# Optimization experiments

Hardware: AMD Instinct MI355X
Metric: run time of the kernel (lower is better)

The kernel has to match this reference:

```python
import jax, jax.numpy as jnp
import numpy as np

NUM_HEADS = 16
EPS = 1e-6

def _rmsnorm(h, w):
    h32 = h.astype(jnp.float32)
    var = jnp.mean(h32 * h32, axis=-1, keepdims=True)
    return (w * (h32 * jax.lax.rsqrt(var + EPS))).astype(h.dtype)

def setup_inputs() -> dict:
    key = jax.random.key(0)
    ks = jax.random.split(key, 4)
    B, N, C = 16, 1024, 1024
    x = jax.random.normal(ks[0], (B, N, C), dtype=jnp.float32)
    qkv_w = jax.random.normal(ks[1], (3 * C, C), dtype=jnp.float32) * (C ** -0.5)
    proj_w = jax.random.normal(ks[2], (C, C), dtype=jnp.float32) * (C ** -0.5)
    proj_b = jnp.zeros((C,), dtype=jnp.float32)
    q_norm_w = jnp.ones((C // NUM_HEADS,), dtype=jnp.float32)
    k_norm_w = jnp.ones((C // NUM_HEADS,), dtype=jnp.float32)
    return {"x": x, "qkv_w": qkv_w, "proj_w": proj_w, "proj_b": proj_b,
            "q_norm_w": q_norm_w, "k_norm_w": k_norm_w}

def reference(x, qkv_w, proj_w, proj_b, q_norm_w, k_norm_w):
    B, N, C = x.shape
    H = NUM_HEADS
    Dh = C // H
    scale = Dh ** -0.5  # qk_scale default; temperature = 1.0
    # QKV projection (no bias): [B,N,3,H,Dh]
    qkv = (x @ qkv_w.T).reshape(B, N, 3, H, Dh)
    q, k, v = qkv[:, :, 0], qkv[:, :, 1], qkv[:, :, 2]
    # per-head QK RMSNorm (fp32 internally)
    q = _rmsnorm(q, q_norm_w)
    k = _rmsnorm(k, k_norm_w)
    # explicit softmax attention: [B,H,N,N]
    attn = jnp.einsum('bnhd,bmhd->bhnm', q * scale, k)
    attn = jax.nn.softmax(attn, axis=-1)
    out = jnp.einsum('bhnm,bmhd->bnhd', attn, v).reshape(B, N, C)
    return out @ proj_w.T + proj_b
```

## Files before the change

### kernel.cpp

```cpp
#include <hip/hip_runtime.h>
#include <hip/hip_bf16.h>

typedef __attribute__((ext_vector_type(8))) __bf16 bf16x8;
typedef __attribute__((ext_vector_type(4))) __bf16 bf16x4;
typedef __attribute__((ext_vector_type(4))) float f32x4;

#define AS1(p) ((__attribute__((address_space(1))) void*)(p))
#define AS3(p) ((__attribute__((address_space(3))) void*)(p))

__global__ void f2b_kernel(const float4* __restrict__ in, bf16x4* __restrict__ out, int n4) {
    int idx = blockIdx.x * blockDim.x + threadIdx.x;
    int stride = gridDim.x * blockDim.x;
    for (int i = idx; i < n4; i += stride) {
        float4 v = in[i];
        bf16x4 o;
        o[0] = (__bf16)v.x; o[1] = (__bf16)v.y; o[2] = (__bf16)v.z; o[3] = (__bf16)v.w;
        out[i] = o;
    }
}

template<int MODE>
__global__ __launch_bounds__(512, 2)
void gemm256(const __bf16* __restrict__ A, const __bf16* __restrict__ Bw,
             const float* __restrict__ bias, const float* __restrict__ qw,
             const float* __restrict__ kw, float* __restrict__ Cf,
             __bf16* __restrict__ Cb, __bf16* __restrict__ Vt,
             int M, int K, int nbn, int ldc)
{
    __shared__ __bf16 Asl[4][256 * 32];
    __shared__ __bf16 Bsl[4][256 * 32];
    const int tid = threadIdx.x, l = tid & 63, w = tid >> 6;
    const int fr = l & 15, fk = l >> 4;

    const int cpx = gridDim.x >> 3;
    const int wg = (blockIdx.x & 7) * cpx + (blockIdx.x >> 3);
    const int bm = wg / nbn, bn = wg % nbn;

    const __bf16* Ag = A + (size_t)bm * 256 * K;
    const __bf16* Bg = Bw + (size_t)bn * 256 * K;

    const int arow = tid >> 2;
    const int uch = (tid & 3) ^ (arow & 3);
    const size_t ga = (size_t)arow * K + uch * 8;
    const size_t ga2 = ga + (size_t)128 * K;

    const int axc = (fk ^ (fr & 3)) * 16;
    int aoff[8], boff[4];
    #pragma unroll
    for (int m = 0; m < 8; ++m)
        aoff[m] = ((w >> 2) * 128 + m * 16 + fr) * 64 + axc;
    #pragma unroll
    for (int n = 0; n < 4; ++n)
        boff[n] = ((w & 3) * 64 + n * 16 + fr) * 64 + axc;

    f32x4 acc[8][4] = {};

#define STAGE256(S) do {                                                                    \
    const int sb_ = (S) & 3;                                                                \
    __builtin_amdgcn_global_load_lds(AS1(Ag + (size_t)(S) * 32 + ga),                       \
        AS3((char*)&Asl[sb_][0] + tid * 16), 16, 0, 0);                                     \
    __builtin_amdgcn_global_load_lds(AS1(Ag + (size_t)(S) * 32 + ga2),                      \
        AS3((char*)&Asl[sb_][0] + tid * 16 + 8192), 16, 0, 0);                              \
    __builtin_amdgcn_global_load_lds(AS1(Bg + (size_t)(S) * 32 + ga),                       \
        AS3((char*)&Bsl[sb_][0] + tid * 16), 16, 0, 0);                                     \
    __builtin_amdgcn_global_load_lds(AS1(Bg + (size_t)(S) * 32 + ga2),                      \
        AS3((char*)&Bsl[sb_][0] + tid * 16 + 8192), 16, 0, 0);                              \
} while (0)

#define PHASE256(S, VMSTR, DOSTAGE) do {                                                    \
    asm volatile("s_waitcnt vmcnt(" VMSTR ")" ::: "memory");                                \
    __builtin_amdgcn_s_barrier();                                                           \
    __builtin_amdgcn_sched_barrier(0);                                                      \
    const int pb_ = (S) & 3;                                                                \
    bf16x8 af[8], bfv[4];                                                                   \
    _Pragma("unroll")                                                                       \
    for (int m = 0; m < 8; ++m)                                                             \
        af[m] = *(const bf16x8*)((const char*)&Asl[pb_][0] + aoff[m]);                      \
    _Pragma("unroll")                                                                       \
    for (int n = 0; n < 4; ++n)                                                             \
        bfv[n] = *(const bf16x8*)((const char*)&Bsl[pb_][0] + boff[n]);                     \
    if (DOSTAGE) STAGE256((S) + 3);                                                         \
    __builtin_amdgcn_s_setprio(1);                                                          \
    _Pragma("unroll")                                                                       \
    for (int m = 0; m < 8; ++m)                                                             \
        _Pragma("unroll")                                                                   \
        for (int n = 0; n < 4; ++n)                                                         \
            acc[m][n] = __builtin_amdgcn_mfma_f32_16x16x32_bf16(af[m], bfv[n], acc[m][n], 0, 0, 0); \
    __builtin_amdgcn_s_setprio(0);                                                          \
} while (0)

    const int S = K >> 5;
    STAGE256(0); STAGE256(1); STAGE256(2);
    for (int s = 0; s < S - 2; ++s)
        PHASE256(s, "8", (s + 3 < S));
    PHASE256(S - 2, "4", false);
    PHASE256(S - 1, "0", false);
#undef PHASE256
#undef STAGE256

    const int rb0 = bm * 256 + (w >> 2) * 128 + fk * 4;
    const int cb0 = bn * 256 + (w & 3) * 64;

    if (MODE == 1) {
        #pragma unroll
        for (int m = 0; m < 8; ++m)
            #pragma unroll
            for (int n = 0; n < 4; ++n) {
                const int col = cb0 + n * 16 + fr;
                const float bv = bias[col];
                #pragma unroll
                for (int r = 0; r < 4; ++r)
                    Cf[(size_t)(rb0 + m * 16 + r) * ldc + col] = acc[m][n][r] + bv;
            }
    } else {
        const int sect = bn >> 2;
        if (sect < 2) {
            const float* wp = (sect == 0) ? qw : kw;
            float wn[4];
            #pragma unroll
            for (int n = 0; n < 4; ++n) wn[n] = wp[((w & 3) * 64 + n * 16 + fr) & 63];
            #pragma unroll
            for (int m = 0; m < 8; ++m) {
                float sc[4];
                #pragma unroll
                for (int r = 0; r < 4; ++r) {
                    float ps = 0.f;
                    #pragma unroll
                    for (int n = 0; n < 4; ++n) ps += acc[m][n][r] * acc[m][n][r];
                    ps += __shfl_xor(ps, 1); ps += __shfl_xor(ps, 2);
                    ps += __shfl_xor(ps, 4); ps += __shfl_xor(ps, 8);
                    sc[r] = rsqrtf(ps * (1.0f / 64.0f) + 1e-6f);
                    if (sect == 0) sc[r] *= 0.18033688011112042f;
                }
                #pragma unroll
                for (int n = 0; n < 4; ++n)
                    #pragma unroll
                    for (int r = 0; r < 4; ++r)
                        Cb[(size_t)(rb0 + m * 16 + r) * ldc + cb0 + n * 16 + fr] =
                            (__bf16)(acc[m][n][r] * sc[r] * wn[n]);
            }
        } else {
            #pragma unroll
            for (int m = 0; m < 8; ++m) {
                const int tok = rb0 + m * 16;
                const int b = tok >> 10, ntok = tok & 1023;
                #pragma unroll
                for (int n = 0; n < 4; ++n) {
                    const int vd = (bn - 8) * 256 + (w & 3) * 64 + n * 16 + fr;
                    bf16x4 pk;
                    #pragma unroll
                    for (int r = 0; r < 4; ++r) pk[r] = (__bf16)acc[m][n][r];
                    *(bf16x4*)&Vt[((size_t)((b * 16 + (vd >> 6)) * 64 + (vd & 63))) * 1024 + ntok] = pk;
                }
            }
        }
    }
}

__global__ __launch_bounds__(256, 3)
void attn_kernel(const __bf16* __restrict__ qkv, const __bf16* __restrict__ vt,
                 __bf16* __restrict__ ao)
{
    __shared__ __bf16 Ks[2][64 * 64];
    __shared__ __bf16 Vs[2][64 * 64];
    __shared__ __bf16 Pl[4][16 * 64];
    const int tid = threadIdx.x, l = tid & 63, w = tid >> 6;
    const int fr = l & 15, fk = l >> 4;
    const int sw = (fr & 7) << 4;

    const int bi = blockIdx.x;
    const int L = (bi & 7) * 256 + (bi >> 3);
    const int qb = L & 7, h = (L >> 3) & 15, b = L >> 7;

    const __bf16* Kg = qkv + (size_t)b * 1024 * 2048 + 1024 + h * 64;
    const __bf16* Vg = vt + (size_t)((b * 16 + h) * 64) * 1024;
    const int srow = tid >> 3, scp = tid & 7;

#define STAGE(KT, BUF) do {                                                               \
    _Pragma("unroll")                                                                     \
    for (int i_ = 0; i_ < 2; ++i_) {                                                      \
        const int row_ = i_ * 32 + srow;                                                  \
        const int c_ = scp ^ (row_ & 7);                                                  \
        __builtin_amdgcn_global_load_lds(AS1(Kg + (size_t)((KT) * 64 + row_) * 2048 + c_ * 8), \
                                         AS3(&Ks[BUF][i_ * 2048 + tid * 8]), 16, 0, 0);   \
        __builtin_amdgcn_global_load_lds(AS1(Vg + (size_t)row_ * 1024 + (KT) * 64 + c_ * 8),   \
                                         AS3(&Vs[BUF][i_ * 2048 + tid * 8]), 16, 0, 0);   \
    } } while (0)

    STAGE(0, 0);

    const int qrow0 = b * 1024 + qb * 128 + w * 32;
    bf16x8 qf[2][2];
    #pragma unroll
    for (int qi = 0; qi < 2; ++qi)
        #pragma unroll
        for (int dc = 0; dc < 2; ++dc)
            qf[qi][dc] = *(const bf16x8*)&qkv[(size_t)(qrow0 + qi * 16 + fr) * 2048
                                              + h * 64 + dc * 32 + fk * 8];

    f32x4 oacc[2][4] = {};
    float lsp[2] = {0.0f, 0.0f};

    char* Pw = (char*)&Pl[w][0];
    __syncthreads();

    for (int kt = 0; kt < 16; ++kt) {
        const int cur = kt & 1;
        if (kt < 15) STAGE(kt + 1, cur ^ 1);

        bf16x8 kf[4][2], vf[4][2];
        #pragma unroll
        for (int n = 0; n < 4; ++n)
            #pragma unroll
            for (int dc = 0; dc < 2; ++dc)
                kf[n][dc] = *(const bf16x8*)&Ks[cur][(n * 16 + fr) * 64
                                                     + (((dc * 4 + fk) ^ (fr & 7)) * 8)];
        #pragma unroll
        for (int nd = 0; nd < 4; ++nd)
            #pragma unroll
            for (int kc = 0; kc < 2; ++kc)
                vf[nd][kc] = *(const bf16x8*)&Vs[cur][(nd * 16 + fr) * 64
                                                      + (((kc * 4 + fk) ^ (fr & 7)) * 8)];

        #pragma unroll
        for (int qi = 0; qi < 2; ++qi) {
            f32x4 sacc[4] = {};
            #pragma unroll
            for (int n = 0; n < 4; ++n)
                #pragma unroll
                for (int dc = 0; dc < 2; ++dc)
                    sacc[n] = __builtin_amdgcn_mfma_f32_16x16x32_bf16(kf[n][dc], qf[qi][dc],
                                                                      sacc[n], 0, 0, 0);

            #pragma unroll
            for (int n = 0; n < 4; ++n) {
                bf16x4 pk;
                #pragma unroll
                for (int r = 0; r < 4; ++r) {
                    float p = exp2f(sacc[n][r]);
                    lsp[qi] += p;
                    pk[r] = (__bf16)p;
                }
                *(bf16x4*)(Pw + ((fr * 128 + n * 32 + fk * 8) ^ sw)) = pk;
            }

            bf16x8 pf[2];
            #pragma unroll
            for (int kc = 0; kc < 2; ++kc)
                pf[kc] = *(const bf16x8*)(Pw + ((fr * 128 + kc * 64 + fk * 16) ^ sw));
            #pragma unroll
            for (int nd = 0; nd < 4; ++nd)
                #pragma unroll
                for (int kc = 0; kc < 2; ++kc)
                    oacc[qi][nd] = __builtin_amdgcn_mfma_f32_16x16x32_bf16(pf[kc], vf[nd][kc],
                                                                           oacc[qi][nd], 0, 0, 0);
        }
        __syncthreads();
    }

    #pragma unroll
    for (int qi = 0; qi < 2; ++qi) {
        float ls = lsp[qi];
        ls += __shfl_xor(ls, 16);
        ls += __shfl_xor(ls, 32);
        float inv[4];
        #pragma unroll
        for (int r = 0; r < 4; ++r)
            inv[r] = __builtin_amdgcn_rcpf(__shfl(ls, (l & 48) + fk * 4 + r));
        #pragma unroll
        for (int nd = 0; nd < 4; ++nd)
            #pragma unroll
            for (int r = 0; r < 4; ++r)
                ao[(size_t)(qrow0 + qi * 16 + fk * 4 + r) * 1024 + h * 64 + nd * 16 + fr] =
                    (__bf16)(oacc[qi][nd][r] * inv[r]);
    }
#undef STAGE
}

extern "C" void kernel_launch(void* const* d_in, const int* in_sizes, int n_in,
                              void* d_out, int out_size, void* d_ws, size_t ws_size,
                              hipStream_t stream)
{
    const float* x      = (const float*)d_in[0];
    const float* qkv_w  = (const float*)d_in[1];
    const float* proj_w = (const float*)d_in[2];
    const float* proj_b = (const float*)d_in[3];
    const float* qnw    = (const float*)d_in[4];
    const float* knw    = (const float*)d_in[5];

    char* ws = (char*)d_ws;
    __bf16* xb    = (__bf16*)(ws);
    __bf16* wqkv  = (__bf16*)(ws + 33554432);
    __bf16* wproj = (__bf16*)(ws + 39845888);
    __bf16* qkv   = (__bf16*)(ws + 41943040);
    __bf16* vt    = (__bf16*)(ws + 109051904);
    __bf16* ao    = (__bf16*)(ws + 142606336);

    f2b_kernel<<<2048, 256, 0, stream>>>((const float4*)x,      (bf16x4*)xb,    16777216 / 4);
    f2b_kernel<<<2048, 256, 0, stream>>>((const float4*)qkv_w,  (bf16x4*)wqkv,  3145728 / 4);
    f2b_kernel<<<1024, 256, 0, stream>>>((const float4*)proj_w, (bf16x4*)wproj, 1048576 / 4);

    gemm256<0><<<768, 512, 0, stream>>>(xb, wqkv, nullptr, qnw, knw,
                                        nullptr, qkv, vt, 16384, 1024, 12, 2048);
    attn_kernel<<<2048, 256, 0, stream>>>(qkv, vt, ao);
    gemm256<1><<<256, 512, 0, stream>>>(ao, wproj, proj_b, nullptr, nullptr,
                                        (float*)d_out, nullptr, nullptr, 16384, 1024, 4, 1024);
}
```

Baseline: 292.2 us.

## Compute softmax row sums via MFMA with ones vector and precompute LDS offsets

The attention kernel stops accumulating the softmax denominator with scalar adds and cross-lane shuffles. It instead runs extra MFMAs that multiply the bf16 probability tile by a ones vector, which gives row sums already laid out like the output accumulator. It also swaps exp2f for the raw hardware exp2 intrinsic and precomputes staging and LDS read/write offsets as pointer increments to cut address arithmetic. The trade is two extra MFMAs per query sub-tile per key tile, and row sums are now taken from bf16-rounded probabilities, which matches what multiplies V.

```diff
diff --git a/kernel.cpp b/kernel.cpp
--- a/kernel.cpp
+++ b/kernel.cpp
@@ -176,18 +176,20 @@
     const __bf16* Vg = vt + (size_t)((b * 16 + h) * 64) * 1024;
     const int srow = tid >> 3, scp = tid & 7;
 
-#define STAGE(KT, BUF) do {                                                               \
-    _Pragma("unroll")                                                                     \
-    for (int i_ = 0; i_ < 2; ++i_) {                                                      \
-        const int row_ = i_ * 32 + srow;                                                  \
-        const int c_ = scp ^ (row_ & 7);                                                  \
-        __builtin_amdgcn_global_load_lds(AS1(Kg + (size_t)((KT) * 64 + row_) * 2048 + c_ * 8), \
-                                         AS3(&Ks[BUF][i_ * 2048 + tid * 8]), 16, 0, 0);   \
-        __builtin_amdgcn_global_load_lds(AS1(Vg + (size_t)row_ * 1024 + (KT) * 64 + c_ * 8),   \
-                                         AS3(&Vs[BUF][i_ * 2048 + tid * 8]), 16, 0, 0);   \
-    } } while (0)
-
-    STAGE(0, 0);
+    const int c8 = (scp ^ (srow & 7)) * 8;
+    const size_t kO0 = (size_t)srow * 2048 + c8, kO1 = kO0 + 32 * 2048;
+    const size_t vO0 = (size_t)srow * 1024 + c8, vO1 = vO0 + 32 * 1024;
+    char* ksd = (char*)&Ks[0][0] + tid * 16;
+    char* vsd = (char*)&Vs[0][0] + tid * 16;
+
+#define STAGE(KP, VP, BUF) do {                                                           \
+    __builtin_amdgcn_global_load_lds(AS1((KP) + kO0), AS3(ksd + (BUF) * 8192), 16, 0, 0); \
+    __builtin_amdgcn_global_load_lds(AS1((KP) + kO1), AS3(ksd + (BUF) * 8192 + 4096), 16, 0, 0); \
+    __builtin_amdgcn_global_load_lds(AS1((VP) + vO0), AS3(vsd + (BUF) * 8192), 16, 0, 0); \
+    __builtin_amdgcn_global_load_lds(AS1((VP) + vO1), AS3(vsd + (BUF) * 8192 + 4096), 16, 0, 0); \
+} while (0)
+
+    STAGE(Kg, Vg, 0);
 
     const int qrow0 = b * 1024 + qb * 128 + w * 32;
     bf16x8 qf[2][2];
@@ -198,29 +200,46 @@
             qf[qi][dc] = *(const bf16x8*)&qkv[(size_t)(qrow0 + qi * 16 + fr) * 2048
                                               + h * 64 + dc * 32 + fk * 8];
 
+    const int kb0 = fr * 128 + ((fk ^ (fr & 7)) * 16);
+    const int kb1 = fr * 128 + (((4 + fk) ^ (fr & 7)) * 16);
+    const char* KsB = (const char*)&Ks[0][0];
+    const char* VsB = (const char*)&Vs[0][0];
+
+    char* Pw = (char*)&Pl[w][0];
+    const int pw0 = (fr * 128 + 0 * 32 + fk * 8) ^ sw;
+    const int pw1 = (fr * 128 + 1 * 32 + fk * 8) ^ sw;
+    const int pw2 = (fr * 128 + 2 * 32 + fk * 8) ^ sw;
+    const int pw3 = (fr * 128 + 3 * 32 + fk * 8) ^ sw;
+    const int pr0 = (fr * 128 + 0 * 64 + fk * 16) ^ sw;
+    const int pr1 = (fr * 128 + 1 * 64 + fk * 16) ^ sw;
+
+    bf16x8 onesf;
+    #pragma unroll
+    for (int i = 0; i < 8; ++i) onesf[i] = (__bf16)1.0f;
+
     f32x4 oacc[2][4] = {};
-    float lsp[2] = {0.0f, 0.0f};
-
-    char* Pw = (char*)&Pl[w][0];
+    f32x4 lacc[2] = {};
+
+    const __bf16* kg = Kg;
+    const __bf16* vg = Vg;
     __syncthreads();
 
     for (int kt = 0; kt < 16; ++kt) {
         const int cur = kt & 1;
-        if (kt < 15) STAGE(kt + 1, cur ^ 1);
-
+        if (kt < 15) { kg += 64 * 2048; vg += 64; STAGE(kg, vg, cur ^ 1); }
+
+        const int cb = cur * 8192;
         bf16x8 kf[4][2], vf[4][2];
         #pragma unroll
-        for (int n = 0; n < 4; ++n)
-            #pragma unroll
-            for (int dc = 0; dc < 2; ++dc)
-                kf[n][dc] = *(const bf16x8*)&Ks[cur][(n * 16 + fr) * 64
-                                                     + (((dc * 4 + fk) ^ (fr & 7)) * 8)];
-        #pragma unroll
-        for (int nd = 0; nd < 4; ++nd)
-            #pragma unroll
-            for (int kc = 0; kc < 2; ++kc)
-                vf[nd][kc] = *(const bf16x8*)&Vs[cur][(nd * 16 + fr) * 64
-                                                      + (((kc * 4 + fk) ^ (fr & 7)) * 8)];
+        for (int n = 0; n < 4; ++n) {
+            kf[n][0] = *(const bf16x8*)(KsB + cb + kb0 + n * 2048);
+            kf[n][1] = *(const bf16x8*)(KsB + cb + kb1 + n * 2048);
+        }
+        #pragma unroll
+        for (int nd = 0; nd < 4; ++nd) {
+            vf[nd][0] = *(const bf16x8*)(VsB + cb + kb0 + nd * 2048);
+            vf[nd][1] = *(const bf16x8*)(VsB + cb + kb1 + nd * 2048);
+        }
 
         #pragma unroll
         for (int qi = 0; qi < 2; ++qi) {
@@ -236,37 +255,33 @@
             for (int n = 0; n < 4; ++n) {
                 bf16x4 pk;
                 #pragma unroll
-                for (int r = 0; r < 4; ++r) {
-                    float p = exp2f(sacc[n][r]);
-                    lsp[qi] += p;
-                    pk[r] = (__bf16)p;
-                }
-                *(bf16x4*)(Pw + ((fr * 128 + n * 32 + fk * 8) ^ sw)) = pk;
-            }
-
-            bf16x8 pf[2];
-            #pragma unroll
-            for (int kc = 0; kc < 2; ++kc)
-                pf[kc] = *(const bf16x8*)(Pw + ((fr * 128 + kc * 64 + fk * 16) ^ sw));
-            #pragma unroll
-            for (int nd = 0; nd < 4; ++nd)
-                #pragma unroll
-                for (int kc = 0; kc < 2; ++kc)
-                    oacc[qi][nd] = __builtin_amdgcn_mfma_f32_16x16x32_bf16(pf[kc], vf[nd][kc],
-                                                                           oacc[qi][nd], 0, 0, 0);
+                for (int r = 0; r < 4; ++r)
+                    pk[r] = (__bf16)__builtin_amdgcn_exp2f(sacc[n][r]);
+                const int pwn = (n == 0) ? pw0 : (n == 1) ? pw1 : (n == 2) ? pw2 : pw3;
+                *(bf16x4*)(Pw + pwn) = pk;
+            }
+
+            bf16x8 pf0 = *(const bf16x8*)(Pw + pr0);
+            bf16x8 pf1 = *(const bf16x8*)(Pw + pr1);
+            lacc[qi] = __builtin_amdgcn_mfma_f32_16x16x32_bf16(pf0, onesf, lacc[qi], 0, 0, 0);
+            lacc[qi] = __builtin_amdgcn_mfma_f32_16x16x32_bf16(pf1, onesf, lacc[qi], 0, 0, 0);
+            #pragma unroll
+            for (int nd = 0; nd < 4; ++nd) {
+                oacc[qi][nd] = __builtin_amdgcn_mfma_f32_16x16x32_bf16(pf0, vf[nd][0],
+                                                                       oacc[qi][nd], 0, 0, 0);
+                oacc[qi][nd] = __builtin_amdgcn_mfma_f32_16x16x32_bf16(pf1, vf[nd][1],
+                                                                       oacc[qi][nd], 0, 0, 0);
+            }
         }
         __syncthreads();
     }
 
     #pragma unroll
     for (int qi = 0; qi < 2; ++qi) {
-        float ls = lsp[qi];
-        ls += __shfl_xor(ls, 16);
-        ls += __shfl_xor(ls, 32);
         float inv[4];
         #pragma unroll
         for (int r = 0; r < 4; ++r)
-            inv[r] = __builtin_amdgcn_rcpf(__shfl(ls, (l & 48) + fk * 4 + r));
+            inv[r] = __builtin_amdgcn_rcpf(lacc[qi][r]);
         #pragma unroll
         for (int nd = 0; nd < 4; ++nd)
             #pragma unroll
```

Result: faster. 268.7 us (-8.0%).
